# Performance work log

Measured on AMD Instinct MI355X. Metric: run time of the kernel, lower is better.

Reference implementation:

```python
import jax, jax.numpy as jnp
import numpy as np

DIM = 96; NH = 3; HD = DIM // NH; SCALE = HD ** -0.5
WS = (7, 7, 7); N = WS[0] * WS[1] * WS[2]
SHIFT = (3, 3, 3)  # half window
NL = 2
GRID = (28, 28, 28)
B = 2


def _rel_index():
    wd, wh, ww = WS
    coords = np.stack(np.meshgrid(np.arange(wd), np.arange(wh), np.arange(ww), indexing='ij')).reshape(3, -1)
    rel = (coords[:, :, None] - coords[:, None, :]).transpose(1, 2, 0)  # [N,N,3]
    rel[..., 0] += wd - 1; rel[..., 1] += wh - 1; rel[..., 2] += ww - 1
    rel[..., 0] *= (2 * wh - 1) * (2 * ww - 1); rel[..., 1] *= (2 * ww - 1)
    return rel.sum(-1)  # [N,N]

REL_IDX = _rel_index()


def _window_partition(x):
    b, D, H, W, C = x.shape
    wd, wh, ww = WS
    x = x.reshape(b, D // wd, wd, H // wh, wh, W // ww, ww, C)
    x = x.transpose(0, 1, 3, 5, 2, 4, 6, 7)
    return x.reshape(-1, N, C)


def _window_reverse(win, b, D, H, W):
    wd, wh, ww = WS
    C = win.shape[-1]
    x = win.reshape(b, D // wd, H // wh, W // ww, wd, wh, ww, C)
    x = x.transpose(0, 1, 4, 2, 5, 3, 6, 7)
    return x.reshape(b, D, H, W, C)


def _compute_mask():
    # MONAI compute_mask for the shifted (SW-MSA) block
    D, H, W = GRID; wd, wh, ww = WS; sd, sh, sw = SHIFT
    img = np.zeros((1, D, H, W, 1), np.float32)
    cnt = 0
    for d in (slice(-wd), slice(-wd, -sd), slice(-sd, None)):
        for h in (slice(-wh), slice(-wh, -sh), slice(-sh, None)):
            for w in (slice(-ww), slice(-ww, -sw), slice(-sw, None)):
                img[:, d, h, w, :] = cnt; cnt += 1
    mw = img.reshape(1, D // wd, wd, H // wh, wh, W // ww, ww, 1)
    mw = mw.transpose(0, 1, 3, 5, 2, 4, 6, 7).reshape(-1, N)  # [nw, N]
    am = mw[:, None, :] - mw[:, :, None]
    return np.where(am != 0, np.float32(-100.0), np.float32(0.0))

MASK = jnp.asarray(_compute_mask())  # [nw, N, N]


def _ln(x, g, b):
    mu = x.mean(-1, keepdims=True)
    var = ((x - mu) ** 2).mean(-1, keepdims=True)
    return (x - mu) / jnp.sqrt(var + 1e-5) * g + b


def _block(x, p, shift, mask):
    b, D, H, W, C = x.shape
    h = _ln(x, p['n1g'], p['n1b'])
    if shift is not None:
        h = jnp.roll(h, (-shift[0], -shift[1], -shift[2]), axis=(1, 2, 3))
    xw = _window_partition(h)  # [b*nw, N, C]
    Bn = xw.shape[0]
    qkv = (xw @ p['qkvw'].T + p['qkvb']).reshape(Bn, N, 3, NH, HD).transpose(2, 0, 3, 1, 4)
    q, k, v = qkv[0] * SCALE, qkv[1], qkv[2]
    attn = jnp.einsum('bhnd,bhmd->bhnm', q, k)
    bias = p['rel'][REL_IDX.reshape(-1)].reshape(N, N, NH).transpose(2, 0, 1)
    attn = attn + bias[None]
    if mask is not None:
        nw = mask.shape[0]
        attn = (attn.reshape(Bn // nw, nw, NH, N, N) + mask[None, :, None]).reshape(Bn, NH, N, N)
    attn = jax.nn.softmax(attn, axis=-1)
    out = jnp.einsum('bhnm,bhmd->bhnd', attn, v).transpose(0, 2, 1, 3).reshape(Bn, N, C)
    out = out @ p['projw'].T + p['projb']
    h = _window_reverse(out, b, D, H, W)
    if shift is not None:
        h = jnp.roll(h, shift, axis=(1, 2, 3))
    x = x + h
    m = _ln(x, p['n2g'], p['n2b'])
    m = jax.nn.gelu(m @ p['fc1w'].T + p['fc1b'], approximate=False) @ p['fc2w'].T + p['fc2b']
    return x + m


def setup_inputs() -> dict:
    key = jax.random.key(0)
    ks = jax.random.split(key, 8)
    nbias = (2 * WS[0] - 1) * (2 * WS[1] - 1) * (2 * WS[2] - 1)
    return {
        'x': jax.random.normal(ks[0], (B,) + GRID + (DIM,), jnp.float32),
        'norm1_g': jnp.ones((NL, DIM), jnp.float32),
        'norm1_b': jnp.zeros((NL, DIM), jnp.float32),
        'qkv_w': jax.random.normal(ks[1], (NL, 3 * DIM, DIM), jnp.float32) * 0.02,
        'qkv_b': jnp.zeros((NL, 3 * DIM), jnp.float32),
        'rel_bias': jax.random.normal(ks[2], (NL, nbias, NH), jnp.float32) * 0.02,
        'proj_w': jax.random.normal(ks[3], (NL, DIM, DIM), jnp.float32) * 0.02,
        'proj_b': jnp.zeros((NL, DIM), jnp.float32),
        'norm2_g': jnp.ones((NL, DIM), jnp.float32),
        'norm2_b': jnp.zeros((NL, DIM), jnp.float32),
        'fc1_w': jax.random.normal(ks[4], (NL, 4 * DIM, DIM), jnp.float32) * 0.02,
        'fc1_b': jnp.zeros((NL, 4 * DIM), jnp.float32),
        'fc2_w': jax.random.normal(ks[5], (NL, DIM, 4 * DIM), jnp.float32) * 0.02,
        'fc2_b': jnp.zeros((NL, DIM), jnp.float32),
    }


def reference(x, norm1_g, norm1_b, qkv_w, qkv_b, rel_bias, proj_w, proj_b,
              norm2_g, norm2_b, fc1_w, fc1_b, fc2_w, fc2_b):
    for i in range(NL):
        p = dict(n1g=norm1_g[i], n1b=norm1_b[i], qkvw=qkv_w[i], qkvb=qkv_b[i],
                 rel=rel_bias[i], projw=proj_w[i], projb=proj_b[i],
                 n2g=norm2_g[i], n2b=norm2_b[i], fc1w=fc1_w[i], fc1b=fc1_b[i],
                 fc2w=fc2_w[i], fc2b=fc2_b[i])
        if i % 2 == 0:
            x = _block(x, p, None, None)  # W-MSA (mask is all-zero for shift=0)
        else:
            x = _block(x, p, SHIFT, MASK)  # SW-MSA
    return x
```

## Files before the change

### kernel.cpp

```cpp
#include <hip/hip_runtime.h>
#include <math.h>

#define DIM 96
#define NHD 3
#define HD 32
#define NWT 343
#define NWIN 128
#define TOK 43904
#define NBIAS 2197
#define SCALE 0.17677669529663687f
#define TPAD 352
#define TSZ  (343 * 352)

typedef __attribute__((ext_vector_type(8))) short bf16x8;
typedef __attribute__((ext_vector_type(4))) float f32x4;

__device__ __forceinline__ unsigned short f2b(float f) {
    union { float f; unsigned int u; } x; x.f = f;
    unsigned int r = (x.u + 0x7fffu + ((x.u >> 16) & 1u)) >> 16;
    return (unsigned short)r;
}
__device__ __forceinline__ unsigned int pk2bf(float a, float b) {
    union { float f; unsigned int u; } x, y; x.f = a; y.f = b;
    return ((x.u + 0x8000u) >> 16) | ((y.u + 0x8000u) & 0xffff0000u);
}
__device__ __forceinline__ float lo16(unsigned int u) {
    union { unsigned int u; float f; } x; x.u = u << 16; return x.f;
}
__device__ __forceinline__ float hi16(unsigned int u) {
    union { unsigned int u; float f; } x; x.u = u & 0xffff0000u; return x.f;
}

__global__ void __launch_bounds__(256) k_cvt4(
        const float* __restrict__ s0, const float* __restrict__ s1,
        const float* __restrict__ s2, const float* __restrict__ s3,
        unsigned short* __restrict__ dst) {
    int i = blockIdx.x * 256 + threadIdx.x;
    if (i >= 221184) return;
    const float* src; int off;
    if (i < 55296)       { src = s0; off = i; }
    else if (i < 73728)  { src = s1; off = i - 55296; }
    else if (i < 147456) { src = s2; off = i - 73728; }
    else                 { src = s3; off = i - 147456; }
    dst[i] = f2b(src[off]);
}

__global__ void __launch_bounds__(256) k_bias(
        const float* __restrict__ rel0, const float* __restrict__ rel1,
        unsigned short* __restrict__ bt) {
    int i = blockIdx.x * 256 + threadIdx.x;
    if (i >= 9 * 3 * TSZ) return;
    int c = i % 352;
    int t = i / 352;
    int q = t % 343; t /= 343;
    int head = t % 3; int combo = t / 3;
    int j = c & 7, q4i = (c >> 3) & 3, pr = c >> 5;
    int kcol = pr * 32 + ((j >> 2) << 4) + q4i * 4 + (j & 3);
    float outv;
    if (kcol >= 343) {
        outv = -100000.0f;
    } else {
        int dq = q / 49, hq = (q / 7) % 7, wq = q % 7;
        int dk = kcol / 49, hk = (kcol / 7) % 7, wk = kcol % 7;
        int ridx = (dq - dk + 6) * 169 + (hq - hk + 6) * 13 + (wq - wk + 6);
        const float* rel = (combo == 0) ? rel0 : rel1;
        float b = rel[ridx * 3 + head];
        if (combo > 0) {
            int ty = combo - 1;
            int rqd = (ty & 4) ? 1 + (dq >= 4) : 0;
            int rqh = (ty & 2) ? 1 + (hq >= 4) : 0;
            int rqw = (ty & 1) ? 1 + (wq >= 4) : 0;
            int rkd = (ty & 4) ? 1 + (dk >= 4) : 0;
            int rkh = (ty & 2) ? 1 + (hk >= 4) : 0;
            int rkw = (ty & 1) ? 1 + (wk >= 4) : 0;
            if (rqd != rkd || rqh != rkh || rqw != rkw) b -= 100.0f;
        }
        outv = b;
    }
    bt[i] = f2b(outv);
}

__global__ void __launch_bounds__(256) k_qkv(
        const float* __restrict__ x, const float* __restrict__ g1,
        const float* __restrict__ b1, const unsigned short* __restrict__ W,
        const float* __restrict__ bias, unsigned short* __restrict__ q,
        unsigned short* __restrict__ k, unsigned short* __restrict__ v, int shift) {
    __shared__ __align__(16) unsigned short lns[64][104];
    __shared__ __align__(16) unsigned short wbuf[96][104];
    int wid = threadIdx.x >> 6, lane = threadIdx.x & 63;
    int lm = lane & 15, q4 = lane >> 4;
    int m0 = blockIdx.x * 64 + wid * 16;
    int bwr[4], nnr[4];
    size_t rowoff[4];
    #pragma unroll
    for (int r = 0; r < 4; ++r) {
        int wtok = m0 + q4 * 4 + r;
        int bw = wtok / NWT, n = wtok % NWT;
        bwr[r] = bw; nnr[r] = n;
        int b = bw >> 6, win = bw & 63;
        int wdi = win >> 4, whi = (win >> 2) & 3, wwi = win & 3;
        int d = n / 49, h = (n / 7) % 7, w = n % 7;
        int sd = (wdi * 7 + d + shift) % 28;
        int sh = (whi * 7 + h + shift) % 28;
        int sw = (wwi * 7 + w + shift) % 28;
        rowoff[r] = (((size_t)(b * 28 + sd) * 28 + sh) * 28 + sw) * 96;
    }
    float val[6][4], g1v[6], b1v[6];
    #pragma unroll
    for (int c = 0; c < 6; ++c) {
        int ncol = c * 16 + lm;
        g1v[c] = g1[ncol]; b1v[c] = b1[ncol];
        #pragma unroll
        for (int r = 0; r < 4; ++r) val[c][r] = x[rowoff[r] + ncol];
    }
    #pragma unroll
    for (int r = 0; r < 4; ++r) {
        float s = 0.f, s2 = 0.f;
        #pragma unroll
        for (int c = 0; c < 6; ++c) { s += val[c][r]; s2 += val[c][r] * val[c][r]; }
        #pragma unroll
        for (int off = 8; off > 0; off >>= 1) {
            s  += __shfl_xor(s,  off, 64);
            s2 += __shfl_xor(s2, off, 64);
        }
        float mu = s * (1.0f / 96.0f);
        float rstd = rsqrtf(s2 * (1.0f / 96.0f) - mu * mu + 1e-5f);
        int row = wid * 16 + q4 * 4 + r;
        #pragma unroll
        for (int c = 0; c < 6; ++c)
            lns[row][c * 16 + lm] = f2b((val[c][r] - mu) * rstd * g1v[c] + b1v[c]);
    }
    __syncthreads();
    bf16x8 a1[3];
    #pragma unroll
    for (int ks = 0; ks < 3; ++ks)
        a1[ks] = *((const bf16x8*)&lns[wid * 16 + lm][ks * 32 + q4 * 8]);
    for (int ch = 0; ch < 3; ++ch) {
        __syncthreads();
        const uint4* src = (const uint4*)(W + ch * 96 * 96);
        for (int s = threadIdx.x; s < 1152; s += 256) {
            int row = s / 12, seg = s % 12;
            *((uint4*)&wbuf[row][seg * 8]) = src[s];
        }
        __syncthreads();
        f32x4 acc[6];
        #pragma unroll
        for (int c = 0; c < 6; ++c) acc[c] = (f32x4){0.f, 0.f, 0.f, 0.f};
        #pragma unroll
        for (int ks = 0; ks < 3; ++ks) {
            #pragma unroll
            for (int c = 0; c < 6; ++c) {
                bf16x8 b = *((const bf16x8*)&wbuf[c * 16 + lm][ks * 32 + q4 * 8]);
                acc[c] = __builtin_amdgcn_mfma_f32_16x16x32_bf16(a1[ks], b, acc[c], 0, 0, 0);
            }
        }
        #pragma unroll
        for (int c = 0; c < 6; ++c) {
            int col = c * 16 + lm;
            int head = col >> 5, hd = col & 31;
            float bb = bias[ch * 96 + col];
            #pragma unroll
            for (int r = 0; r < 4; ++r) {
                int wh = bwr[r] * NHD + head;
                float vv = acc[c][r] + bb;
                if (ch == 0)
                    q[(size_t)wh * (TPAD * 32) + nnr[r] * 32 + hd] = f2b(vv * SCALE);
                else if (ch == 1)
                    k[(size_t)wh * (TPAD * 32) + nnr[r] * 32 + hd] = f2b(vv);
                else
                    v[(size_t)wh * (32 * TPAD) + hd * TPAD + nnr[r]] = f2b(vv);
            }
        }
    }
}

__global__ void __launch_bounds__(256) k_attn(
        const unsigned short* __restrict__ q, const unsigned short* __restrict__ k,
        const unsigned short* __restrict__ vT, const unsigned short* __restrict__ bt,
        unsigned short* __restrict__ o, int tmul) {
    __shared__ __align__(16) unsigned short vts[32 * 360];
    __shared__ __align__(16) unsigned short pbuf[4][2][16 * 40];
    int wh = blockIdx.x / 3, third = blockIdx.x % 3;
    int bw = wh / NHD, head = wh % NHD;
    const unsigned int* vsrc = (const unsigned int*)(vT + (size_t)wh * 32 * TPAD);
    unsigned int* vdst = (unsigned int*)vts;
    for (int i = threadIdx.x; i < 32 * 176; i += 256) {
        int row = i / 176, cc = i - row * 176;
        vdst[row * 180 + cc] = vsrc[i];
    }
    __syncthreads();
    int win = bw & 63;
    int wdi = win >> 4, whi = (win >> 2) & 3, wwi = win & 3;
    int type = ((wdi == 3) ? 4 : 0) | ((whi == 3) ? 2 : 0) | ((wwi == 3) ? 1 : 0);
    const unsigned short* bbase = bt + (size_t)type * tmul + (size_t)head * TSZ;
    int wid = threadIdx.x >> 6, lane = threadIdx.x & 63;
    int lm = lane & 15, q4 = lane >> 4;
    int tb = third * 8 + wid * 2;
    if (tb > 21) return;
    bool dual = (tb + 1 <= 21);
    int qtA = tb, qtB = dual ? tb + 1 : tb;
    const unsigned short* qbase = q + (size_t)wh * TPAD * 32;
    const unsigned short* kbase = k + (size_t)wh * TPAD * 32;
    int qtokA = qtA * 16 + lm, qtokB = qtB * 16 + lm;
    bf16x8 qfA = *((const bf16x8*)(qbase + qtokA * 32 + q4 * 8));
    bf16x8 qfB = *((const bf16x8*)(qbase + qtokB * 32 + q4 * 8));
    const unsigned short* bpA = bbase + (size_t)min(qtokA, NWT - 1) * 352;
    const unsigned short* bpB = bbase + (size_t)min(qtokB, NWT - 1) * 352;
    f32x4 aA0 = (f32x4){0.f,0.f,0.f,0.f}, aA1 = aA0, aB0 = aA0, aB1 = aA0;
    float dA = 0.f, dB = 0.f;
    unsigned short* pbA = pbuf[wid][0];
    unsigned short* pbB = pbuf[wid][1];
    bf16x8 kf0n = *((const bf16x8*)(kbase + lm * 32 + q4 * 8));
    bf16x8 kf1n = *((const bf16x8*)(kbase + (16 + lm) * 32 + q4 * 8));
    uint4 bAn = *((const uint4*)(bpA + q4 * 8));
    uint4 bBn = *((const uint4*)(bpB + q4 * 8));
    for (int pr = 0; pr < 11; ++pr) {
        int kb0 = pr * 32;
        bf16x8 kf0 = kf0n, kf1 = kf1n;
        uint4 uA = bAn, uB = bBn;
        if (pr < 10) {
            int kb1 = kb0 + 32;
            kf0n = *((const bf16x8*)(kbase + (kb1 + lm) * 32 + q4 * 8));
            kf1n = *((const bf16x8*)(kbase + (kb1 + 16 + lm) * 32 + q4 * 8));
            bAn = *((const uint4*)(bpA + kb1 + q4 * 8));
            bBn = *((const uint4*)(bpB + kb1 + q4 * 8));
        }
        f32x4 z = (f32x4){0.f, 0.f, 0.f, 0.f};
        f32x4 sA0 = __builtin_amdgcn_mfma_f32_16x16x32_bf16(kf0, qfA, z, 0, 0, 0);
        f32x4 sA1 = __builtin_amdgcn_mfma_f32_16x16x32_bf16(kf1, qfA, z, 0, 0, 0);
        f32x4 sB0 = __builtin_amdgcn_mfma_f32_16x16x32_bf16(kf0, qfB, z, 0, 0, 0);
        f32x4 sB1 = __builtin_amdgcn_mfma_f32_16x16x32_bf16(kf1, qfB, z, 0, 0, 0);
        float pA[8], pB[8];
        pA[0] = __expf(sA0[0] + lo16(uA.x)); pA[1] = __expf(sA0[1] + hi16(uA.x));
        pA[2] = __expf(sA0[2] + lo16(uA.y)); pA[3] = __expf(sA0[3] + hi16(uA.y));
        pA[4] = __expf(sA1[0] + lo16(uA.z)); pA[5] = __expf(sA1[1] + hi16(uA.z));
        pA[6] = __expf(sA1[2] + lo16(uA.w)); pA[7] = __expf(sA1[3] + hi16(uA.w));
        pB[0] = __expf(sB0[0] + lo16(uB.x)); pB[1] = __expf(sB0[1] + hi16(uB.x));
        pB[2] = __expf(sB0[2] + lo16(uB.y)); pB[3] = __expf(sB0[3] + hi16(uB.y));
        pB[4] = __expf(sB1[0] + lo16(uB.z)); pB[5] = __expf(sB1[1] + hi16(uB.z));
        pB[6] = __expf(sB1[2] + lo16(uB.w)); pB[7] = __expf(sB1[3] + hi16(uB.w));
        #pragma unroll
        for (int j = 0; j < 8; ++j) { dA += pA[j]; dB += pB[j]; }
        #pragma unroll
        for (int t = 0; t < 2; ++t) {
            *((unsigned int*)(pbA + lm * 40 + t * 16 + q4 * 4)) =
                pk2bf(pA[t * 4 + 0], pA[t * 4 + 1]);
            *((unsigned int*)(pbA + lm * 40 + t * 16 + q4 * 4 + 2)) =
                pk2bf(pA[t * 4 + 2], pA[t * 4 + 3]);
            *((unsigned int*)(pbB + lm * 40 + t * 16 + q4 * 4)) =
                pk2bf(pB[t * 4 + 0], pB[t * 4 + 1]);
            *((unsigned int*)(pbB + lm * 40 + t * 16 + q4 * 4 + 2)) =
                pk2bf(pB[t * 4 + 2], pB[t * 4 + 3]);
        }
        bf16x8 pfA = *((const bf16x8*)(pbA + lm * 40 + q4 * 8));
        bf16x8 pfB = *((const bf16x8*)(pbB + lm * 40 + q4 * 8));
        bf16x8 v0 = *((const bf16x8*)(vts + lm * 360 + kb0 + q4 * 8));
        bf16x8 v1 = *((const bf16x8*)(vts + (16 + lm) * 360 + kb0 + q4 * 8));
        aA0 = __builtin_amdgcn_mfma_f32_16x16x32_bf16(pfA, v0, aA0, 0, 0, 0);
        aA1 = __builtin_amdgcn_mfma_f32_16x16x32_bf16(pfA, v1, aA1, 0, 0, 0);
        aB0 = __builtin_amdgcn_mfma_f32_16x16x32_bf16(pfB, v0, aB0, 0, 0, 0);
        aB1 = __builtin_amdgcn_mfma_f32_16x16x32_bf16(pfB, v1, aB1, 0, 0, 0);
    }
    dA += __shfl_xor(dA, 16, 64); dA += __shfl_xor(dA, 32, 64);
    dB += __shfl_xor(dB, 16, 64); dB += __shfl_xor(dB, 32, 64);
    #pragma unroll
    for (int r = 0; r < 4; ++r) {
        int qrowA = qtA * 16 + q4 * 4 + r;
        if (qrowA < NWT) {
            float inv = 1.0f / __shfl(dA, q4 * 4 + r, 64);
            unsigned short* op = o + (size_t)(bw * NWT + qrowA) * DIM + head * HD;
            op[lm]      = f2b(aA0[r] * inv);
            op[16 + lm] = f2b(aA1[r] * inv);
        }
    }
    if (dual) {
        #pragma unroll
        for (int r = 0; r < 4; ++r) {
            int qrowB = qtB * 16 + q4 * 4 + r;
            if (qrowB < NWT) {
                float inv = 1.0f / __shfl(dB, q4 * 4 + r, 64);
                unsigned short* op = o + (size_t)(bw * NWT + qrowB) * DIM + head * HD;
                op[lm]      = f2b(aB0[r] * inv);
                op[16 + lm] = f2b(aB1[r] * inv);
            }
        }
    }
}

__global__ void __launch_bounds__(256) k_pm(
        const unsigned short* __restrict__ ao, const unsigned short* __restrict__ Wp,
        const float* __restrict__ pbias, const float* __restrict__ xin,
        float* __restrict__ xout,
        const float* __restrict__ g2, const float* __restrict__ b2,
        const unsigned short* __restrict__ w1, const float* __restrict__ bb1,
        const unsigned short* __restrict__ w2, const float* __restrict__ bb2,
        int shift) {
    __shared__ __align__(16) unsigned short lns[64][104];
    __shared__ __align__(16) unsigned short big[18816];
    int wid = threadIdx.x >> 6, lane = threadIdx.x & 63;
    int lm = lane & 15, q4 = lane >> 4;
    int m0 = blockIdx.x * 64 + wid * 16;
    for (int s = threadIdx.x; s < 1152; s += 256) {
        int row = s / 12, seg = s % 12;
        *((uint4*)&big[row * 104 + seg * 8]) = ((const uint4*)Wp)[s];
    }
    const unsigned short* arow = ao + (size_t)(m0 + lm) * 96;
    bf16x8 a1[3];
    #pragma unroll
    for (int ks = 0; ks < 3; ++ks)
        a1[ks] = *((const bf16x8*)(arow + ks * 32 + q4 * 8));
    __syncthreads();
    f32x4 acc[6];
    #pragma unroll
    for (int c = 0; c < 6; ++c) acc[c] = (f32x4){0.f, 0.f, 0.f, 0.f};
    #pragma unroll
    for (int ks = 0; ks < 3; ++ks) {
        #pragma unroll
        for (int c = 0; c < 6; ++c) {
            bf16x8 b = *((const bf16x8*)&big[(c * 16 + lm) * 104 + ks * 32 + q4 * 8]);
            acc[c] = __builtin_amdgcn_mfma_f32_16x16x32_bf16(a1[ks], b, acc[c], 0, 0, 0);
        }
    }
    size_t rowoff[4];
    #pragma unroll
    for (int r = 0; r < 4; ++r) {
        int wtok = m0 + q4 * 4 + r;
        int bw = wtok / NWT, n = wtok % NWT;
        int b = bw >> 6, win = bw & 63;
        int wdi = win >> 4, whi = (win >> 2) & 3, wwi = win & 3;
        int d = n / 49, h = (n / 7) % 7, w = n % 7;
        int sd = (wdi * 7 + d + shift) % 28;
        int sh = (whi * 7 + h + shift) % 28;
        int sw = (wwi * 7 + w + shift) % 28;
        rowoff[r] = (((size_t)(b * 28 + sd) * 28 + sh) * 28 + sw) * 96;
    }
    float val[6][4], g2v[6], b2v[6];
    #pragma unroll
    for (int c = 0; c < 6; ++c) {
        int n = c * 16 + lm;
        float bb = pbias[n];
        g2v[c] = g2[n]; b2v[c] = b2[n];
        #pragma unroll
        for (int r = 0; r < 4; ++r)
            val[c][r] = xin[rowoff[r] + n] + acc[c][r] + bb;
    }
    #pragma unroll
    for (int r = 0; r < 4; ++r) {
        float s = 0.f, s2 = 0.f;
        #pragma unroll
        for (int c = 0; c < 6; ++c) { s += val[c][r]; s2 += val[c][r] * val[c][r]; }
        #pragma unroll
        for (int off = 8; off > 0; off >>= 1) {
            s  += __shfl_xor(s,  off, 64);
            s2 += __shfl_xor(s2, off, 64);
        }
        float mu = s * (1.0f / 96.0f);
        float rstd = rsqrtf(s2 * (1.0f / 96.0f) - mu * mu + 1e-5f);
        int row = wid * 16 + q4 * 4 + r;
        #pragma unroll
        for (int c = 0; c < 6; ++c)
            lns[row][c * 16 + lm] = f2b((val[c][r] - mu) * rstd * g2v[c] + b2v[c]);
    }
    bf16x8 am[3];
    #pragma unroll
    for (int ks = 0; ks < 3; ++ks)
        am[ks] = *((const bf16x8*)&lns[wid * 16 + lm][ks * 32 + q4 * 8]);
    f32x4 acc2[6];
    #pragma unroll
    for (int c = 0; c < 6; ++c) acc2[c] = (f32x4){0.f, 0.f, 0.f, 0.f};
    unsigned short* hid_ = &big[13952 + wid * 1216];
    for (int ch = 0; ch < 6; ++ch) {
        __syncthreads();
        const uint4* src1 = (const uint4*)(w1 + ch * 64 * 96);
        #pragma unroll
        for (int t = 0; t < 3; ++t) {
            int s = threadIdx.x + t * 256;
            int row = s / 12, seg = s % 12;
            *((uint4*)&big[row * 104 + seg * 8]) = src1[s];
        }
        #pragma unroll
        for (int t = 0; t < 3; ++t) {
            int s = threadIdx.x + t * 256;
            int row = s >> 3, seg = s & 7;
            *((uint4*)&big[6656 + row * 76 + seg * 8]) =
                *((const uint4*)(w2 + row * 384 + ch * 64 + seg * 8));
        }
        __syncthreads();
        f32x4 acc1[4];
        #pragma unroll
        for (int t = 0; t < 4; ++t) acc1[t] = (f32x4){0.f, 0.f, 0.f, 0.f};
        #pragma unroll
        for (int ks = 0; ks < 3; ++ks) {
            #pragma unroll
            for (int t = 0; t < 4; ++t) {
                bf16x8 b = *((const bf16x8*)&big[(t * 16 + lm) * 104 + ks * 32 + q4 * 8]);
                acc1[t] = __builtin_amdgcn_mfma_f32_16x16x32_bf16(am[ks], b, acc1[t], 0, 0, 0);
            }
        }
        #pragma unroll
        for (int t = 0; t < 4; ++t) {
            float bb = bb1[ch * 64 + t * 16 + lm];
            #pragma unroll
            for (int r = 0; r < 4; ++r) {
                float v2 = acc1[t][r] + bb;
                float ge = 0.5f * v2 * (1.0f + erff(v2 * 0.70710678118654752f));
                hid_[(q4 * 4 + r) * 76 + t * 16 + lm] = f2b(ge);
            }
        }
        #pragma unroll
        for (int ks2 = 0; ks2 < 2; ++ks2) {
            bf16x8 a = *((const bf16x8*)(hid_ + lm * 76 + ks2 * 32 + q4 * 8));
            #pragma unroll
            for (int c = 0; c < 6; ++c) {
                bf16x8 b = *((const bf16x8*)&big[6656 + (c * 16 + lm) * 76 + ks2 * 32 + q4 * 8]);
                acc2[c] = __builtin_amdgcn_mfma_f32_16x16x32_bf16(a, b, acc2[c], 0, 0, 0);
            }
        }
    }
    #pragma unroll
    for (int c = 0; c < 6; ++c) {
        int n = c * 16 + lm;
        float bb = bb2[n];
        #pragma unroll
        for (int r = 0; r < 4; ++r)
            xout[rowoff[r] + n] = val[c][r] + acc2[c][r] + bb;
    }
}

extern "C" void kernel_launch(void* const* d_in, const int* in_sizes, int n_in,
                              void* d_out, int out_size, void* d_ws, size_t ws_size,
                              hipStream_t stream) {
    const float* x     = (const float*)d_in[0];
    const float* n1g   = (const float*)d_in[1];
    const float* n1b   = (const float*)d_in[2];
    const float* qkvw  = (const float*)d_in[3];
    const float* qkvb  = (const float*)d_in[4];
    const float* relb  = (const float*)d_in[5];
    const float* projw = (const float*)d_in[6];
    const float* projb = (const float*)d_in[7];
    const float* n2g   = (const float*)d_in[8];
    const float* n2b   = (const float*)d_in[9];
    const float* fc1w  = (const float*)d_in[10];
    const float* fc1b  = (const float*)d_in[11];
    const float* fc2w  = (const float*)d_in[12];
    const float* fc2b  = (const float*)d_in[13];
    float* out = (float*)d_out;

    const size_t NEL = (size_t)TOK * DIM;
    const size_t QKN = (size_t)NWIN * NHD * TPAD * 32;
    float* buf_x = (float*)d_ws;
    unsigned short* hbuf = (unsigned short*)(buf_x + NEL);
    unsigned short* bq   = hbuf + NEL;
    unsigned short* bk   = bq + QKN;
    unsigned short* bv   = bk + QKN;
    unsigned short* wts  = bv + QKN;
    unsigned short* wq  = wts;
    unsigned short* wp  = wq + 2 * 27648;
    unsigned short* w1  = wp + 2 * 9216;
    unsigned short* w2  = w1 + 2 * 36864;
    unsigned short* btab = wts + 221184;

    k_cvt4<<<(221184 + 255) / 256, 256, 0, stream>>>(qkvw, projw, fc1w, fc2w, wts);
    k_bias<<<(9 * 3 * TSZ + 255) / 256, 256, 0, stream>>>(
        relb, relb + NBIAS * NHD, btab);

    for (int L = 0; L < 2; ++L) {
        int shift = (L == 0) ? 0 : 3;
        const float* xin_l = (L == 0) ? x : buf_x;
        float* xfin = (L == 0) ? buf_x : out;
        const unsigned short* btL = (L == 0) ? btab : btab + 3 * TSZ;
        int tmul = (L == 0) ? 0 : 3 * TSZ;

        k_qkv<<<TOK / 64, 256, 0, stream>>>(xin_l, n1g + L * 96, n1b + L * 96,
                                            wq + L * 27648, qkvb + L * 288,
                                            bq, bk, bv, shift);
        k_attn<<<NWIN * NHD * 3, 256, 0, stream>>>(bq, bk, bv, btL, hbuf, tmul);
        k_pm<<<TOK / 64, 256, 0, stream>>>(hbuf, wp + L * 9216, projb + L * 96,
                                           xin_l, xfin,
                                           n2g + L * 96, n2b + L * 96,
                                           w1 + L * 36864, fc1b + L * 384,
                                           w2 + L * 36864, fc2b + L * 96, shift);
    }
}
```

Measured before the change: 261.4 us.

## Tile bias table per query tile for coalesced loads; approximate GELU with tanh-exp

New measurement: 266.4 us. No clear change (+1.9%).

```diff
diff --git a/kernel.cpp b/kernel.cpp
--- a/kernel.cpp
+++ b/kernel.cpp
@@ -10,7 +10,8 @@
 #define NBIAS 2197
 #define SCALE 0.17677669529663687f
 #define TPAD 352
-#define TSZ  (343 * 352)
+#define QTS 5632
+#define HSZ (22 * QTS)
 
 typedef __attribute__((ext_vector_type(8))) short bf16x8;
 typedef __attribute__((ext_vector_type(4))) float f32x4;
@@ -49,12 +50,13 @@
         const float* __restrict__ rel0, const float* __restrict__ rel1,
         unsigned short* __restrict__ bt) {
     int i = blockIdx.x * 256 + threadIdx.x;
-    if (i >= 9 * 3 * TSZ) return;
-    int c = i % 352;
-    int t = i / 352;
-    int q = t % 343; t /= 343;
+    if (i >= 27 * HSZ) return;
+    int off = i % QTS;
+    int t = i / QTS;
+    int qt = t % 22; t /= 22;
     int head = t % 3; int combo = t / 3;
-    int j = c & 7, q4i = (c >> 3) & 3, pr = c >> 5;
+    int j = off & 7, q4i = (off >> 3) & 3, lm = (off >> 5) & 15, pr = off >> 9;
+    int q = min(qt * 16 + lm, 342);
     int kcol = pr * 32 + ((j >> 2) << 4) + q4i * 4 + (j & 3);
     float outv;
     if (kcol >= 343) {
@@ -192,7 +194,7 @@
     int win = bw & 63;
     int wdi = win >> 4, whi = (win >> 2) & 3, wwi = win & 3;
     int type = ((wdi == 3) ? 4 : 0) | ((whi == 3) ? 2 : 0) | ((wwi == 3) ? 1 : 0);
-    const unsigned short* bbase = bt + (size_t)type * tmul + (size_t)head * TSZ;
+    const unsigned short* bbase = bt + (size_t)type * tmul + (size_t)head * HSZ;
     int wid = threadIdx.x >> 6, lane = threadIdx.x & 63;
     int lm = lane & 15, q4 = lane >> 4;
     int tb = third * 8 + wid * 2;
@@ -204,16 +206,16 @@
     int qtokA = qtA * 16 + lm, qtokB = qtB * 16 + lm;
     bf16x8 qfA = *((const bf16x8*)(qbase + qtokA * 32 + q4 * 8));
     bf16x8 qfB = *((const bf16x8*)(qbase + qtokB * 32 + q4 * 8));
-    const unsigned short* bpA = bbase + (size_t)min(qtokA, NWT - 1) * 352;
-    const unsigned short* bpB = bbase + (size_t)min(qtokB, NWT - 1) * 352;
+    const unsigned short* bpA = bbase + (size_t)qtA * QTS + lm * 32 + q4 * 8;
+    const unsigned short* bpB = bbase + (size_t)qtB * QTS + lm * 32 + q4 * 8;
     f32x4 aA0 = (f32x4){0.f,0.f,0.f,0.f}, aA1 = aA0, aB0 = aA0, aB1 = aA0;
     float dA = 0.f, dB = 0.f;
     unsigned short* pbA = pbuf[wid][0];
     unsigned short* pbB = pbuf[wid][1];
     bf16x8 kf0n = *((const bf16x8*)(kbase + lm * 32 + q4 * 8));
     bf16x8 kf1n = *((const bf16x8*)(kbase + (16 + lm) * 32 + q4 * 8));
-    uint4 bAn = *((const uint4*)(bpA + q4 * 8));
-    uint4 bBn = *((const uint4*)(bpB + q4 * 8));
+    uint4 bAn = *((const uint4*)bpA);
+    uint4 bBn = *((const uint4*)bpB);
     for (int pr = 0; pr < 11; ++pr) {
         int kb0 = pr * 32;
         bf16x8 kf0 = kf0n, kf1 = kf1n;
@@ -222,8 +224,8 @@
             int kb1 = kb0 + 32;
             kf0n = *((const bf16x8*)(kbase + (kb1 + lm) * 32 + q4 * 8));
             kf1n = *((const bf16x8*)(kbase + (kb1 + 16 + lm) * 32 + q4 * 8));
-            bAn = *((const uint4*)(bpA + kb1 + q4 * 8));
-            bBn = *((const uint4*)(bpB + kb1 + q4 * 8));
+            bAn = *((const uint4*)(bpA + (pr + 1) * 512));
+            bBn = *((const uint4*)(bpB + (pr + 1) * 512));
         }
         f32x4 z = (f32x4){0.f, 0.f, 0.f, 0.f};
         f32x4 sA0 = __builtin_amdgcn_mfma_f32_16x16x32_bf16(kf0, qfA, z, 0, 0, 0);
@@ -403,7 +405,10 @@
             #pragma unroll
             for (int r = 0; r < 4; ++r) {
                 float v2 = acc1[t][r] + bb;
-                float ge = 0.5f * v2 * (1.0f + erff(v2 * 0.70710678118654752f));
+                float t2 = v2 * v2;
+                float m = fmaf(-0.0713548162f, t2, -1.5957691216f);
+                float e = __expf(v2 * m);
+                float ge = v2 * (1.0f / (1.0f + e));
                 hid_[(q4 * 4 + r) * 76 + t * 16 + lm] = f2b(ge);
             }
         }
@@ -461,15 +466,15 @@
     unsigned short* btab = wts + 221184;
 
     k_cvt4<<<(221184 + 255) / 256, 256, 0, stream>>>(qkvw, projw, fc1w, fc2w, wts);
-    k_bias<<<(9 * 3 * TSZ + 255) / 256, 256, 0, stream>>>(
+    k_bias<<<(27 * HSZ + 255) / 256, 256, 0, stream>>>(
         relb, relb + NBIAS * NHD, btab);
 
     for (int L = 0; L < 2; ++L) {
         int shift = (L == 0) ? 0 : 3;
         const float* xin_l = (L == 0) ? x : buf_x;
         float* xfin = (L == 0) ? buf_x : out;
-        const unsigned short* btL = (L == 0) ? btab : btab + 3 * TSZ;
-        int tmul = (L == 0) ? 0 : 3 * TSZ;
+        const unsigned short* btL = (L == 0) ? btab : btab + 3 * HSZ;
+        int tmul = (L == 0) ? 0 : 3 * HSZ;
 
         k_qkv<<<TOK / 64, 256, 0, stream>>>(xin_l, n1g + L * 96, n1b + L * 96,
                                             wq + L * 27648, qkvb + L * 288,
```
